# Kernel optimization log

Measured on AMD Instinct MI355X. Metric: run time of the kernel, lower is better.

Reference implementation:

```python
import jax, jax.numpy as jnp
import numpy as np

B, S, H = 2, 2048, 2048
NH, NKV, D = 32, 8, 64
N_REP = NH // NKV  # 4
THETA = 10000.0


def _rotate_half(x):
    x1, x2 = jnp.split(x, 2, axis=-1)
    return jnp.concatenate([-x2, x1], axis=-1)


def _apply_rope(q, k, position_ids):
    # q: [B,NH,S,D], k: [B,NKV,S,D], position_ids: [B,S]
    inv_freq = 1.0 / (THETA ** (jnp.arange(0, D, 2, dtype=jnp.float32) / D))  # [D/2]
    ang = position_ids[:, None, :, None].astype(jnp.float32) * inv_freq      # [B,1,S,D/2]
    cos = jnp.concatenate([jnp.cos(ang), jnp.cos(ang)], axis=-1)             # [B,1,S,D]
    sin = jnp.concatenate([jnp.sin(ang), jnp.sin(ang)], axis=-1)
    q = q * cos + _rotate_half(q) * sin
    k = k * cos + _rotate_half(k) * sin
    return q, k


def setup_inputs() -> dict:
    key = jax.random.key(0)
    k1, k2, k3, k4 = jax.random.split(key, 4)
    hidden_states = jax.random.normal(k1, (B, S, H), dtype=jnp.float32)
    position_ids = jnp.broadcast_to(jnp.arange(S, dtype=jnp.int64 if jax.config.jax_enable_x64 else jnp.int32)[None, :], (B, S))
    Wq = jax.random.normal(k2, (H, NH * D), dtype=jnp.float32) * 0.02
    Wkv = jax.random.normal(k3, (H, NKV * 2 * D), dtype=jnp.float32) * 0.02
    Wo = jax.random.normal(k4, (H, H), dtype=jnp.float32) * 0.02
    return {"hidden_states": hidden_states, "position_ids": position_ids,
            "Wq": Wq, "Wkv": Wkv, "Wo": Wo}


def reference(hidden_states, position_ids, Wq, Wkv, Wo):
    b, s, _ = hidden_states.shape
    # fused QKV projections (Linear, no bias)
    q = (hidden_states @ Wq).reshape(b, s, NH, D).transpose(0, 2, 1, 3)      # [B,NH,S,D]
    kv = (hidden_states @ Wkv).reshape(b, s, NKV, 2, D)
    k = kv[:, :, :, 0, :].transpose(0, 2, 1, 3)                              # [B,NKV,S,D]
    v = kv[:, :, :, 1, :].transpose(0, 2, 1, 3)                              # [B,NKV,S,D]
    # rotary embedding
    q, k = _apply_rope(q, k, position_ids)
    # GQA: repeat_interleave K/V heads
    k = jnp.repeat(k, N_REP, axis=1)                                         # [B,NH,S,D]
    v = jnp.repeat(v, N_REP, axis=1)
    # causal SDPA (eval mode: dropout_p = 0)
    scale = 1.0 / np.sqrt(D)
    scores = jnp.einsum('bhqd,bhkd->bhqk', q, k) * scale                     # [B,NH,S,S]
    causal = jnp.tril(jnp.ones((s, s), dtype=bool))
    scores = jnp.where(causal[None, None], scores, jnp.finfo(scores.dtype).min)
    probs = jax.nn.softmax(scores, axis=-1)
    ctx = jnp.einsum('bhqk,bhkd->bhqd', probs, v)                            # [B,NH,S,D]
    ctx = ctx.transpose(0, 2, 1, 3).reshape(b, s, H)
    return ctx @ Wo
```

## Files before the change

kernel.cpp:

```cpp
#include <hip/hip_runtime.h>

typedef __bf16 bf16_t;
typedef __bf16 bf16x8 __attribute__((ext_vector_type(8)));
typedef __bf16 bf16x4 __attribute__((ext_vector_type(4)));
typedef float f32x4 __attribute__((ext_vector_type(4)));

#define DEV static __device__ __forceinline__

DEV void gload16(const void* g, void* lds) {
  __builtin_amdgcn_global_load_lds((__attribute__((address_space(1))) void*)g,
                                   (__attribute__((address_space(3))) void*)lds, 16, 0, 0);
}

DEV f32x4 mfma16(bf16x8 a, bf16x8 b, f32x4 c) {
  return __builtin_amdgcn_mfma_f32_16x16x32_bf16(a, b, c, 0, 0, 0);
}

__global__ __launch_bounds__(256) void k_cvt_bf16(const float* __restrict__ in,
                                                  bf16_t* __restrict__ out, int n) {
  int i = (blockIdx.x * 256 + threadIdx.x) * 4;
  if (i + 3 < n) {
    float4 v = *(const float4*)(in + i);
    bf16x4 o;
    o[0] = (bf16_t)v.x; o[1] = (bf16_t)v.y; o[2] = (bf16_t)v.z; o[3] = (bf16_t)v.w;
    *(bf16x4*)(out + i) = o;
  }
}

__global__ __launch_bounds__(256) void k_transpose(const float* __restrict__ in,
                                                   bf16_t* __restrict__ out, int R, int C) {
  __shared__ float tile[32][33];
  const int tx = threadIdx.x & 31, ty = threadIdx.x >> 5;
  const int rb = blockIdx.y * 32, cb = blockIdx.x * 32;
#pragma unroll
  for (int i = 0; i < 32; i += 8)
    tile[ty + i][tx] = in[(size_t)(rb + ty + i) * C + (cb + tx)];
  __syncthreads();
#pragma unroll
  for (int i = 0; i < 32; i += 8)
    out[(size_t)(cb + ty + i) * R + (rb + tx)] = (bf16_t)tile[tx][ty + i];
}

__global__ __launch_bounds__(256) void k_rope_table(const int* __restrict__ pos_ids,
                                                    float2* __restrict__ tbl) {
  const int token = blockIdx.x * 8 + (threadIdx.x >> 5);
  const int d2 = threadIdx.x & 31;
  const float p = (float)pos_ids[token];
  const float freq = exp2f(-(float)d2 / 32.0f * log2f(10000.0f));
  const float a = p * freq;
  tbl[token * 32 + d2] = make_float2(cosf(a), sinf(a));
}

__global__ __launch_bounds__(256) void k_gemm_bt(const bf16_t* __restrict__ A,
                                                 const bf16_t* __restrict__ Bt,
                                                 float* __restrict__ C,
                                                 int M, int N, int K,
                                                 int lda, int ldb, int ldc) {
  __shared__ __align__(16) bf16_t As[128 * 32];
  __shared__ __align__(16) bf16_t Bs[128 * 32];
  const int tid = threadIdx.x;
  const int lane = tid & 63, w = tid >> 6;
  const int c15 = lane & 15, g = lane >> 4;
  const int wr = w >> 1, wc = w & 1;
  const int brow = blockIdx.y * 128, bcol = blockIdx.x * 128;
  const int swzr = (c15 >> 1) & 3;

  const f32x4 fzero = {0.f, 0.f, 0.f, 0.f};
  f32x4 acc[4][4];
#pragma unroll
  for (int m = 0; m < 4; ++m)
#pragma unroll
    for (int n = 0; n < 4; ++n) acc[m][n] = fzero;

  for (int kt = 0; kt < K; kt += 32) {
    __syncthreads();
#pragma unroll
    for (int i = 0; i < 2; ++i) {
      const int c = tid + i * 256;
      const int row = c >> 2, pc = c & 3;
      const int lc = pc ^ ((row >> 1) & 3);
      gload16(A + (size_t)(brow + row) * lda + kt + lc * 8,
              As + (size_t)(w * 64 + i * 256) * 8);
      gload16(Bt + (size_t)(bcol + row) * ldb + kt + lc * 8,
              Bs + (size_t)(w * 64 + i * 256) * 8);
    }
    __syncthreads();
    bf16x8 af[4], bfm[4];
#pragma unroll
    for (int m = 0; m < 4; ++m) {
      const int row = wr * 64 + m * 16 + c15;
      af[m] = *(const bf16x8*)(As + row * 32 + (g ^ swzr) * 8);
    }
#pragma unroll
    for (int n = 0; n < 4; ++n) {
      const int row = wc * 64 + n * 16 + c15;
      bfm[n] = *(const bf16x8*)(Bs + row * 32 + (g ^ swzr) * 8);
    }
#pragma unroll
    for (int m = 0; m < 4; ++m)
#pragma unroll
      for (int n = 0; n < 4; ++n)
        acc[m][n] = mfma16(af[m], bfm[n], acc[m][n]);
  }
#pragma unroll
  for (int m = 0; m < 4; ++m)
#pragma unroll
    for (int n = 0; n < 4; ++n)
#pragma unroll
      for (int r = 0; r < 4; ++r) {
        const int row = brow + wr * 64 + m * 16 + g * 4 + r;
        const int col = bcol + wc * 64 + n * 16 + c15;
        C[(size_t)row * ldc + col] = acc[m][n][r];
      }
}

__global__ __launch_bounds__(256) void k_gemm_qkv(const bf16_t* __restrict__ A,
                                                  const bf16_t* __restrict__ Bt,
                                                  const float2* __restrict__ tbl,
                                                  bf16_t* __restrict__ Qp,
                                                  bf16_t* __restrict__ Kp,
                                                  bf16_t* __restrict__ Vt) {
  __shared__ __align__(16) bf16_t As[128 * 32];
  __shared__ __align__(16) bf16_t Bs[128 * 32];
  const int tid = threadIdx.x;
  const int lane = tid & 63, w = tid >> 6;
  const int c15 = lane & 15, g = lane >> 4;
  const int wr = w >> 1, wc = w & 1;
  const int brow = blockIdx.y * 128, bcol = blockIdx.x * 128;
  const int swzr = (c15 >> 1) & 3;

  const f32x4 fzero = {0.f, 0.f, 0.f, 0.f};
  f32x4 acc[4][4];
#pragma unroll
  for (int m = 0; m < 4; ++m)
#pragma unroll
    for (int n = 0; n < 4; ++n) acc[m][n] = fzero;

  for (int kt = 0; kt < 2048; kt += 32) {
    __syncthreads();
#pragma unroll
    for (int i = 0; i < 2; ++i) {
      const int c = tid + i * 256;
      const int row = c >> 2, pc = c & 3;
      const int lc = pc ^ ((row >> 1) & 3);
      gload16(A + (size_t)(brow + row) * 2048 + kt + lc * 8,
              As + (size_t)(w * 64 + i * 256) * 8);
      gload16(Bt + (size_t)(bcol + row) * 2048 + kt + lc * 8,
              Bs + (size_t)(w * 64 + i * 256) * 8);
    }
    __syncthreads();
    bf16x8 af[4], bfm[4];
#pragma unroll
    for (int m = 0; m < 4; ++m) {
      const int row = wr * 64 + m * 16 + c15;
      af[m] = *(const bf16x8*)(As + row * 32 + (g ^ swzr) * 8);
    }
#pragma unroll
    for (int n = 0; n < 4; ++n) {
      const int row = wc * 64 + n * 16 + c15;
      bfm[n] = *(const bf16x8*)(Bs + row * 32 + (g ^ swzr) * 8);
    }
#pragma unroll
    for (int m = 0; m < 4; ++m)
#pragma unroll
      for (int n = 0; n < 4; ++n)
        acc[m][n] = mfma16(af[m], bfm[n], acc[m][n]);
  }

  const int seg = bcol + wc * 64;
  const int wrow = brow + wr * 64;
  const float QSCALE = 0.125f * 1.44269504088896340736f;

  if (seg < 2048) {
    const int hq = seg >> 6;
#pragma unroll
    for (int m = 0; m < 4; ++m)
#pragma unroll
      for (int r = 0; r < 4; ++r) {
        const int row = wrow + m * 16 + g * 4 + r;
        const int bb = row >> 11, s = row & 2047;
        const float2 cs0 = tbl[row * 32 + c15];
        const float2 cs1 = tbl[row * 32 + 16 + c15];
        bf16_t* dst = Qp + (((size_t)bb * 32 + hq) * 2048 + s) * 64;
        dst[c15]      = (bf16_t)((acc[m][0][r] * cs0.x - acc[m][2][r] * cs0.y) * QSCALE);
        dst[32 + c15] = (bf16_t)((acc[m][2][r] * cs0.x + acc[m][0][r] * cs0.y) * QSCALE);
        dst[16 + c15] = (bf16_t)((acc[m][1][r] * cs1.x - acc[m][3][r] * cs1.y) * QSCALE);
        dst[48 + c15] = (bf16_t)((acc[m][3][r] * cs1.x + acc[m][1][r] * cs1.y) * QSCALE);
      }
  } else {
    const int cc = seg - 2048;
    const int kvh = cc >> 7;
    if (((cc >> 6) & 1) == 0) {
#pragma unroll
      for (int m = 0; m < 4; ++m)
#pragma unroll
        for (int r = 0; r < 4; ++r) {
          const int row = wrow + m * 16 + g * 4 + r;
          const int bb = row >> 11, s = row & 2047;
          const float2 cs0 = tbl[row * 32 + c15];
          const float2 cs1 = tbl[row * 32 + 16 + c15];
          bf16_t* dst = Kp + (((size_t)bb * 8 + kvh) * 2048 + s) * 64;
          dst[c15]      = (bf16_t)(acc[m][0][r] * cs0.x - acc[m][2][r] * cs0.y);
          dst[32 + c15] = (bf16_t)(acc[m][2][r] * cs0.x + acc[m][0][r] * cs0.y);
          dst[16 + c15] = (bf16_t)(acc[m][1][r] * cs1.x - acc[m][3][r] * cs1.y);
          dst[48 + c15] = (bf16_t)(acc[m][3][r] * cs1.x + acc[m][1][r] * cs1.y);
        }
    } else {
#pragma unroll
      for (int m = 0; m < 4; ++m) {
        const int row0 = wrow + m * 16 + g * 4;
        const int bb = row0 >> 11, s0 = row0 & 2047;
#pragma unroll
        for (int n = 0; n < 4; ++n) {
          bf16x4 o;
#pragma unroll
          for (int r = 0; r < 4; ++r) o[r] = (bf16_t)acc[m][n][r];
          const int d = n * 16 + c15;
          *(bf16x4*)(Vt + ((size_t)(bb * 8 + kvh) * 64 + d) * 2048 + s0) = o;
        }
      }
    }
  }
}

__global__ __launch_bounds__(256, 3) void k_attn(const bf16_t* __restrict__ Qp,
                                                 const bf16_t* __restrict__ Kp,
                                                 const bf16_t* __restrict__ Vt,
                                                 bf16_t* __restrict__ ctx) {
  const int wgid = blockIdx.x;
  const int gidx = wgid & 15;
  const int j    = wgid >> 4;
  const int b = gidx >> 3, kvh = gidx & 7;
  const int qs = 63 - j;
  const int tid = threadIdx.x, lane = tid & 63, w = tid >> 6;
  const int h = kvh * 4 + w;
  const int c15 = lane & 15, g = lane >> 4;

  __shared__ __align__(16) bf16_t Ks[2][64 * 64];
  __shared__ __align__(16) bf16_t Vs[2][64 * 64];
  __shared__ __align__(16) bf16_t Pw[4][32 * 64];
  bf16_t* pw = &Pw[w][0];

  const int q0 = qs * 32;

  bf16x8 aq[2][2];
#pragma unroll
  for (int m = 0; m < 2; ++m) {
    const bf16_t* Qrow = Qp + (((size_t)b * 32 + h) * 2048 + q0 + m * 16 + c15) * 64;
    aq[m][0] = *(const bf16x8*)(Qrow + g * 8);
    aq[m][1] = *(const bf16x8*)(Qrow + 32 + g * 8);
  }
  asm volatile("s_waitcnt vmcnt(0)" ::: "memory");

  const bf16_t* Kb = Kp + ((size_t)b * 8 + kvh) * (size_t)(2048 * 64);
  const bf16_t* Vb = Vt + ((size_t)b * 8 + kvh) * (size_t)(64 * 2048);

  const int c0 = tid,      r0 = c0 >> 3, l0 = (c0 & 7) ^ (r0 & 7);
  const int c1 = tid + 256, r1 = c1 >> 3, l1 = (c1 & 7) ^ (r1 & 7);
  const int dst0 = (w * 64) * 8, dst1 = (w * 64 + 256) * 8;

  const f32x4 fzero = {0.f, 0.f, 0.f, 0.f};
  f32x4 acc[2][4];
  f32x4 lsum[2];
#pragma unroll
  for (int m = 0; m < 2; ++m) {
    lsum[m] = fzero;
#pragma unroll
    for (int n = 0; n < 4; ++n) acc[m][n] = fzero;
  }
  bf16x8 bones;
#pragma unroll
  for (int j2 = 0; j2 < 8; ++j2) bones[j2] = (bf16_t)1.0f;

  const int ntw = qs / 2 + 1;

  gload16(Kb + (size_t)r0 * 64 + l0 * 8, &Ks[0][dst0]);
  gload16(Kb + (size_t)r1 * 64 + l1 * 8, &Ks[0][dst1]);
  gload16(Vb + (size_t)r0 * 2048 + l0 * 8, &Vs[0][dst0]);
  gload16(Vb + (size_t)r1 * 2048 + l1 * 8, &Vs[0][dst1]);

  for (int t = 0; t < ntw; ++t) {
    const int kvbase = t * 64;
    const int tnb = (t + 1 < ntw ? t + 1 : t) * 64;
    const int nb = (t + 1) & 1, cb = t & 1;

    gload16(Kb + (size_t)(tnb + r0) * 64 + l0 * 8, &Ks[nb][dst0]);
    gload16(Kb + (size_t)(tnb + r1) * 64 + l1 * 8, &Ks[nb][dst1]);
    gload16(Vb + (size_t)r0 * 2048 + tnb + l0 * 8, &Vs[nb][dst0]);
    gload16(Vb + (size_t)r1 * 2048 + tnb + l1 * 8, &Vs[nb][dst1]);
    asm volatile("s_waitcnt vmcnt(4)" ::: "memory");
    __builtin_amdgcn_s_barrier();

    const bf16_t* Kc = &Ks[cb][0];
    f32x4 sv[2][4];
    __builtin_amdgcn_s_setprio(1);
#pragma unroll
    for (int n = 0; n < 4; ++n) {
      const int row = n * 16 + c15;
      const bf16x8 bk0 = *(const bf16x8*)(Kc + row * 64 + ((g ^ (row & 7)) << 3));
      const bf16x8 bk1 = *(const bf16x8*)(Kc + row * 64 + (((4 + g) ^ (row & 7)) << 3));
      sv[0][n] = mfma16(aq[0][1], bk1, mfma16(aq[0][0], bk0, fzero));
      sv[1][n] = mfma16(aq[1][1], bk1, mfma16(aq[1][0], bk0, fzero));
    }
    __builtin_amdgcn_s_setprio(0);

    if (kvbase + 63 > q0) {
#pragma unroll
      for (int n = 0; n < 4; ++n)
#pragma unroll
        for (int r = 0; r < 4; ++r) {
          const int col = kvbase + n * 16 + c15;
          if (col > q0 + g * 4 + r)      sv[0][n][r] = -1e30f;
          if (col > q0 + 16 + g * 4 + r) sv[1][n][r] = -1e30f;
        }
    }
#pragma unroll
    for (int n = 0; n < 4; ++n)
#pragma unroll
      for (int r = 0; r < 4; ++r) {
        const int col = n * 16 + c15;
        const int rp0 = g * 4 + r, rp1 = 16 + g * 4 + r;
        pw[rp0 * 64 + ((((col >> 3) ^ (rp0 & 7)) << 3) | (col & 7))] = (bf16_t)exp2f(sv[0][n][r]);
        pw[rp1 * 64 + ((((col >> 3) ^ (rp1 & 7)) << 3) | (col & 7))] = (bf16_t)exp2f(sv[1][n][r]);
      }
    asm volatile("s_waitcnt lgkmcnt(0)" ::: "memory");
    __builtin_amdgcn_sched_barrier(0);

    bf16x8 ap[2][2];
#pragma unroll
    for (int m = 0; m < 2; ++m) {
      const int q = m * 16 + c15;
      ap[m][0] = *(const bf16x8*)(pw + q * 64 + ((g ^ (q & 7)) << 3));
      ap[m][1] = *(const bf16x8*)(pw + q * 64 + (((4 + g) ^ (q & 7)) << 3));
    }
    const bf16_t* Vc = &Vs[cb][0];
    __builtin_amdgcn_s_setprio(1);
#pragma unroll
    for (int m = 0; m < 2; ++m)
      lsum[m] = mfma16(ap[m][1], bones, mfma16(ap[m][0], bones, lsum[m]));
#pragma unroll
    for (int n = 0; n < 4; ++n) {
      const int row = n * 16 + c15;
      const bf16x8 bv0 = *(const bf16x8*)(Vc + row * 64 + ((g ^ (row & 7)) << 3));
      const bf16x8 bv1 = *(const bf16x8*)(Vc + row * 64 + (((4 + g) ^ (row & 7)) << 3));
#pragma unroll
      for (int m = 0; m < 2; ++m)
        acc[m][n] = mfma16(ap[m][1], bv1, mfma16(ap[m][0], bv0, acc[m][n]));
    }
    __builtin_amdgcn_s_setprio(0);
    __builtin_amdgcn_s_barrier();
  }

#pragma unroll
  for (int m = 0; m < 2; ++m) {
    float inv[4];
#pragma unroll
    for (int r = 0; r < 4; ++r) inv[r] = 1.0f / lsum[m][r];
#pragma unroll
    for (int n = 0; n < 4; ++n)
#pragma unroll
      for (int r = 0; r < 4; ++r) {
        const int rowq = q0 + m * 16 + g * 4 + r;
        const int col = h * 64 + n * 16 + c15;
        ctx[((size_t)b * 2048 + rowq) * 2048 + col] = (bf16_t)(acc[m][n][r] * inv[r]);
      }
  }
}

extern "C" void kernel_launch(void* const* d_in, const int* in_sizes, int n_in,
                              void* d_out, int out_size, void* d_ws, size_t ws_size,
                              hipStream_t stream) {
  const float* hs  = (const float*)d_in[0];
  const int*   pos = (const int*)d_in[1];
  const float* Wq  = (const float*)d_in[2];
  const float* Wkv = (const float*)d_in[3];
  const float* Wo  = (const float*)d_in[4];
  float* out = (float*)d_out;
  (void)in_sizes; (void)n_in; (void)out_size; (void)ws_size;

  char* p = (char*)d_ws;
  bf16_t* Xbf   = (bf16_t*)p; p += (size_t)4096 * 2048 * 2;
  bf16_t* Wqkvt = (bf16_t*)p; p += (size_t)3072 * 2048 * 2;
  bf16_t* Wot   = (bf16_t*)p; p += (size_t)2048 * 2048 * 2;
  float2* tbl   = (float2*)p; p += (size_t)4096 * 32 * 8;
  bf16_t* Qp    = (bf16_t*)p; p += (size_t)2 * 32 * 2048 * 64 * 2;
  bf16_t* Kp    = (bf16_t*)p; p += (size_t)2 * 8 * 2048 * 64 * 2;
  bf16_t* Vt    = (bf16_t*)p; p += (size_t)2 * 8 * 64 * 2048 * 2;
  bf16_t* ctx   = (bf16_t*)p; p += (size_t)4096 * 2048 * 2;

  k_cvt_bf16<<<8192, 256, 0, stream>>>(hs, Xbf, 4096 * 2048);
  k_transpose<<<dim3(64, 64), 256, 0, stream>>>(Wq, Wqkvt, 2048, 2048);
  k_transpose<<<dim3(32, 64), 256, 0, stream>>>(Wkv, Wqkvt + (size_t)2048 * 2048, 2048, 1024);
  k_transpose<<<dim3(64, 64), 256, 0, stream>>>(Wo, Wot, 2048, 2048);
  k_rope_table<<<512, 256, 0, stream>>>(pos, tbl);
  k_gemm_qkv<<<dim3(24, 32), 256, 0, stream>>>(Xbf, Wqkvt, tbl, Qp, Kp, Vt);
  k_attn<<<1024, 256, 0, stream>>>(Qp, Kp, Vt, ctx);
  k_gemm_bt<<<dim3(16, 32), 256, 0, stream>>>(ctx, Wot, out,
                                              4096, 2048, 2048, 2048, 2048, 2048);
}
```

Measured before the change: 232.4 us.

## Replace GEMMs with 256x256 double-buffered, phase-scheduled MFMA kernel

Both projection GEMMs (QKV with fused RoPE epilogue, and output projection) move to one templated 256x256-tile, 512-thread kernel. It uses 64-wide K stages, double-buffered LDS, async global-to-LDS prefetch two stages ahead, s_setprio/barrier phasing, and XCD-aware block remapping. The aim is to cut global traffic per FLOP and hide load latency behind MFMA work. In exchange it uses more registers and LDS and launches fewer blocks (192 and 128), which may underfill the 256 CUs.

```diff
diff --git a/kernel.cpp b/kernel.cpp
--- a/kernel.cpp
+++ b/kernel.cpp
@@ -51,172 +51,187 @@
   tbl[token * 32 + d2] = make_float2(cosf(a), sinf(a));
 }
 
-__global__ __launch_bounds__(256) void k_gemm_bt(const bf16_t* __restrict__ A,
-                                                 const bf16_t* __restrict__ Bt,
-                                                 float* __restrict__ C,
-                                                 int M, int N, int K,
-                                                 int lda, int ldb, int ldc) {
-  __shared__ __align__(16) bf16_t As[128 * 32];
-  __shared__ __align__(16) bf16_t Bs[128 * 32];
+#define STAGE_A(bi, st, h)                                                      \
+  do {                                                                          \
+    const bf16_t* _s = gA + (size_t)(brow + (h) * 128 + r0) * gK + (st) * 64 + l0 * 8; \
+    gload16(_s, &As[bi][((h) * 1024 + tid) * 8]);                               \
+    gload16(_s + (size_t)64 * gK, &As[bi][((h) * 1024 + 512 + tid) * 8]);       \
+  } while (0)
+
+#define STAGE_B(bi, st, h)                                                      \
+  do {                                                                          \
+    const bf16_t* _s = gB + (size_t)(bcol + (h) * 128 + r0) * gK + (st) * 64 + l0 * 8; \
+    gload16(_s, &Bs[bi][((h) * 1024 + tid) * 8]);                               \
+    gload16(_s + (size_t)64 * gK, &Bs[bi][((h) * 1024 + 512 + tid) * 8]);       \
+  } while (0)
+
+#define LOADA(bi, mh)                                                           \
+  _Pragma("unroll")                                                             \
+  for (int mq = 0; mq < 4; ++mq) {                                              \
+    const int R = wm * 128 + (mh) * 64 + mq * 16 + c15;                         \
+    af[mq][0] = *(const bf16x8*)(&As[bi][(R * 8 + (g ^ (R & 7))) * 8]);         \
+    af[mq][1] = *(const bf16x8*)(&As[bi][(R * 8 + ((4 + g) ^ (R & 7))) * 8]);   \
+  }
+
+#define LOADB(bi, nh)                                                           \
+  _Pragma("unroll")                                                             \
+  for (int nq = 0; nq < 2; ++nq) {                                              \
+    const int R = wn * 64 + ((nh) * 2 + nq) * 16 + c15;                         \
+    bfr[nq][0] = *(const bf16x8*)(&Bs[bi][(R * 8 + (g ^ (R & 7))) * 8]);        \
+    bfr[nq][1] = *(const bf16x8*)(&Bs[bi][(R * 8 + ((4 + g) ^ (R & 7))) * 8]);  \
+  }
+
+#define MFMAQ(mh, nh)                                                           \
+  _Pragma("unroll")                                                             \
+  for (int nq = 0; nq < 2; ++nq)                                                \
+    _Pragma("unroll")                                                           \
+    for (int mq = 0; mq < 4; ++mq)                                              \
+      acc[(mh) * 4 + mq][(nh) * 2 + nq] =                                       \
+          mfma16(af[mq][1], bfr[nq][1],                                         \
+                 mfma16(af[mq][0], bfr[nq][0], acc[(mh) * 4 + mq][(nh) * 2 + nq]));
+
+#define PH_MID()                                            \
+  __builtin_amdgcn_s_barrier();                             \
+  asm volatile("s_waitcnt lgkmcnt(0)" ::: "memory");        \
+  __builtin_amdgcn_sched_barrier(0);                        \
+  __builtin_amdgcn_s_setprio(1)
+
+#define PH_END()                                            \
+  __builtin_amdgcn_s_setprio(0);                            \
+  __builtin_amdgcn_s_barrier()
+
+template <int MODE>
+__global__ __launch_bounds__(512, 2) void k_gemm256(
+    const bf16_t* __restrict__ gA, const bf16_t* __restrict__ gB,
+    int gK, int NBX,
+    float* __restrict__ C, int ldc,
+    const float2* __restrict__ tbl,
+    bf16_t* __restrict__ Qp, bf16_t* __restrict__ Kp, bf16_t* __restrict__ Vt) {
+  __shared__ __align__(16) bf16_t As[2][256 * 64];
+  __shared__ __align__(16) bf16_t Bs[2][256 * 64];
   const int tid = threadIdx.x;
   const int lane = tid & 63, w = tid >> 6;
   const int c15 = lane & 15, g = lane >> 4;
-  const int wr = w >> 1, wc = w & 1;
-  const int brow = blockIdx.y * 128, bcol = blockIdx.x * 128;
-  const int swzr = (c15 >> 1) & 3;
+  const int wm = w >> 2, wn = w & 3;
+
+  const int cpx = (int)gridDim.x >> 3;
+  const int u = ((int)blockIdx.x & 7) * cpx + ((int)blockIdx.x >> 3);
+  const int bx = u % NBX, by = u / NBX;
+  const int brow = by * 256, bcol = bx * 256;
+
+  const int r0 = tid >> 3, p0 = tid & 7;
+  const int l0 = p0 ^ (r0 & 7);
 
   const f32x4 fzero = {0.f, 0.f, 0.f, 0.f};
-  f32x4 acc[4][4];
-#pragma unroll
-  for (int m = 0; m < 4; ++m)
+  f32x4 acc[8][4];
+#pragma unroll
+  for (int m = 0; m < 8; ++m)
 #pragma unroll
     for (int n = 0; n < 4; ++n) acc[m][n] = fzero;
 
-  for (int kt = 0; kt < K; kt += 32) {
-    __syncthreads();
-#pragma unroll
-    for (int i = 0; i < 2; ++i) {
-      const int c = tid + i * 256;
-      const int row = c >> 2, pc = c & 3;
-      const int lc = pc ^ ((row >> 1) & 3);
-      gload16(A + (size_t)(brow + row) * lda + kt + lc * 8,
-              As + (size_t)(w * 64 + i * 256) * 8);
-      gload16(Bt + (size_t)(bcol + row) * ldb + kt + lc * 8,
-              Bs + (size_t)(w * 64 + i * 256) * 8);
-    }
-    __syncthreads();
-    bf16x8 af[4], bfm[4];
-#pragma unroll
-    for (int m = 0; m < 4; ++m) {
-      const int row = wr * 64 + m * 16 + c15;
-      af[m] = *(const bf16x8*)(As + row * 32 + (g ^ swzr) * 8);
-    }
-#pragma unroll
-    for (int n = 0; n < 4; ++n) {
-      const int row = wc * 64 + n * 16 + c15;
-      bfm[n] = *(const bf16x8*)(Bs + row * 32 + (g ^ swzr) * 8);
-    }
-#pragma unroll
-    for (int m = 0; m < 4; ++m)
+  const int NT = gK >> 6;
+
+  STAGE_A(0, 0, 0); STAGE_A(0, 0, 1); STAGE_B(0, 0, 0); STAGE_B(0, 0, 1);
+  STAGE_A(1, 1, 0);
+  asm volatile("s_waitcnt vmcnt(2)" ::: "memory");
+  __builtin_amdgcn_s_barrier();
+
+  for (int t = 0; t < NT; ++t) {
+    const int bi = t & 1, oi = bi ^ 1;
+    const int st1 = (t + 1 < NT) ? t + 1 : NT - 1;
+    const int st2 = (t + 2 < NT) ? t + 2 : NT - 1;
+    bf16x8 af[4][2], bfr[2][2];
+
+    LOADA(bi, 0);
+    LOADB(bi, 0);
+    STAGE_A(oi, st1, 1);
+    STAGE_B(oi, st1, 0);
+    PH_MID();
+    MFMAQ(0, 0);
+    PH_END();
+
+    LOADB(bi, 1);
+    STAGE_B(oi, st1, 1);
+    PH_MID();
+    MFMAQ(0, 1);
+    PH_END();
+
+    LOADA(bi, 1);
+    LOADB(bi, 0);
+    PH_MID();
+    MFMAQ(1, 0);
+    PH_END();
+
+    LOADB(bi, 1);
+    STAGE_A(bi, st2, 0);
+    asm volatile("s_waitcnt vmcnt(2)" ::: "memory");
+    PH_MID();
+    MFMAQ(1, 1);
+    PH_END();
+  }
+
+  if constexpr (MODE == 0) {
+#pragma unroll
+    for (int m = 0; m < 8; ++m)
 #pragma unroll
       for (int n = 0; n < 4; ++n)
-        acc[m][n] = mfma16(af[m], bfm[n], acc[m][n]);
-  }
-#pragma unroll
-  for (int m = 0; m < 4; ++m)
-#pragma unroll
-    for (int n = 0; n < 4; ++n)
-#pragma unroll
-      for (int r = 0; r < 4; ++r) {
-        const int row = brow + wr * 64 + m * 16 + g * 4 + r;
-        const int col = bcol + wc * 64 + n * 16 + c15;
-        C[(size_t)row * ldc + col] = acc[m][n][r];
-      }
-}
-
-__global__ __launch_bounds__(256) void k_gemm_qkv(const bf16_t* __restrict__ A,
-                                                  const bf16_t* __restrict__ Bt,
-                                                  const float2* __restrict__ tbl,
-                                                  bf16_t* __restrict__ Qp,
-                                                  bf16_t* __restrict__ Kp,
-                                                  bf16_t* __restrict__ Vt) {
-  __shared__ __align__(16) bf16_t As[128 * 32];
-  __shared__ __align__(16) bf16_t Bs[128 * 32];
-  const int tid = threadIdx.x;
-  const int lane = tid & 63, w = tid >> 6;
-  const int c15 = lane & 15, g = lane >> 4;
-  const int wr = w >> 1, wc = w & 1;
-  const int brow = blockIdx.y * 128, bcol = blockIdx.x * 128;
-  const int swzr = (c15 >> 1) & 3;
-
-  const f32x4 fzero = {0.f, 0.f, 0.f, 0.f};
-  f32x4 acc[4][4];
-#pragma unroll
-  for (int m = 0; m < 4; ++m)
-#pragma unroll
-    for (int n = 0; n < 4; ++n) acc[m][n] = fzero;
-
-  for (int kt = 0; kt < 2048; kt += 32) {
-    __syncthreads();
-#pragma unroll
-    for (int i = 0; i < 2; ++i) {
-      const int c = tid + i * 256;
-      const int row = c >> 2, pc = c & 3;
-      const int lc = pc ^ ((row >> 1) & 3);
-      gload16(A + (size_t)(brow + row) * 2048 + kt + lc * 8,
-              As + (size_t)(w * 64 + i * 256) * 8);
-      gload16(Bt + (size_t)(bcol + row) * 2048 + kt + lc * 8,
-              Bs + (size_t)(w * 64 + i * 256) * 8);
-    }
-    __syncthreads();
-    bf16x8 af[4], bfm[4];
-#pragma unroll
-    for (int m = 0; m < 4; ++m) {
-      const int row = wr * 64 + m * 16 + c15;
-      af[m] = *(const bf16x8*)(As + row * 32 + (g ^ swzr) * 8);
-    }
-#pragma unroll
-    for (int n = 0; n < 4; ++n) {
-      const int row = wc * 64 + n * 16 + c15;
-      bfm[n] = *(const bf16x8*)(Bs + row * 32 + (g ^ swzr) * 8);
-    }
-#pragma unroll
-    for (int m = 0; m < 4; ++m)
-#pragma unroll
-      for (int n = 0; n < 4; ++n)
-        acc[m][n] = mfma16(af[m], bfm[n], acc[m][n]);
-  }
-
-  const int seg = bcol + wc * 64;
-  const int wrow = brow + wr * 64;
-  const float QSCALE = 0.125f * 1.44269504088896340736f;
-
-  if (seg < 2048) {
-    const int hq = seg >> 6;
-#pragma unroll
-    for (int m = 0; m < 4; ++m)
-#pragma unroll
-      for (int r = 0; r < 4; ++r) {
-        const int row = wrow + m * 16 + g * 4 + r;
-        const int bb = row >> 11, s = row & 2047;
-        const float2 cs0 = tbl[row * 32 + c15];
-        const float2 cs1 = tbl[row * 32 + 16 + c15];
-        bf16_t* dst = Qp + (((size_t)bb * 32 + hq) * 2048 + s) * 64;
-        dst[c15]      = (bf16_t)((acc[m][0][r] * cs0.x - acc[m][2][r] * cs0.y) * QSCALE);
-        dst[32 + c15] = (bf16_t)((acc[m][2][r] * cs0.x + acc[m][0][r] * cs0.y) * QSCALE);
-        dst[16 + c15] = (bf16_t)((acc[m][1][r] * cs1.x - acc[m][3][r] * cs1.y) * QSCALE);
-        dst[48 + c15] = (bf16_t)((acc[m][3][r] * cs1.x + acc[m][1][r] * cs1.y) * QSCALE);
-      }
+#pragma unroll
+        for (int r = 0; r < 4; ++r) {
+          const int row = brow + wm * 128 + m * 16 + g * 4 + r;
+          const int col = bcol + wn * 64 + n * 16 + c15;
+          C[(size_t)row * ldc + col] = acc[m][n][r];
+        }
   } else {
-    const int cc = seg - 2048;
-    const int kvh = cc >> 7;
-    if (((cc >> 6) & 1) == 0) {
-#pragma unroll
-      for (int m = 0; m < 4; ++m)
+    const int seg = bcol + wn * 64;
+    const int wrow = brow + wm * 128;
+    const float QSCALE = 0.125f * 1.44269504088896340736f;
+    if (seg < 2048) {
+      const int hq = seg >> 6;
+#pragma unroll
+      for (int m = 0; m < 8; ++m)
 #pragma unroll
         for (int r = 0; r < 4; ++r) {
           const int row = wrow + m * 16 + g * 4 + r;
           const int bb = row >> 11, s = row & 2047;
           const float2 cs0 = tbl[row * 32 + c15];
           const float2 cs1 = tbl[row * 32 + 16 + c15];
-          bf16_t* dst = Kp + (((size_t)bb * 8 + kvh) * 2048 + s) * 64;
-          dst[c15]      = (bf16_t)(acc[m][0][r] * cs0.x - acc[m][2][r] * cs0.y);
-          dst[32 + c15] = (bf16_t)(acc[m][2][r] * cs0.x + acc[m][0][r] * cs0.y);
-          dst[16 + c15] = (bf16_t)(acc[m][1][r] * cs1.x - acc[m][3][r] * cs1.y);
-          dst[48 + c15] = (bf16_t)(acc[m][3][r] * cs1.x + acc[m][1][r] * cs1.y);
+          bf16_t* dst = Qp + (((size_t)bb * 32 + hq) * 2048 + s) * 64;
+          dst[c15]      = (bf16_t)((acc[m][0][r] * cs0.x - acc[m][2][r] * cs0.y) * QSCALE);
+          dst[32 + c15] = (bf16_t)((acc[m][2][r] * cs0.x + acc[m][0][r] * cs0.y) * QSCALE);
+          dst[16 + c15] = (bf16_t)((acc[m][1][r] * cs1.x - acc[m][3][r] * cs1.y) * QSCALE);
+          dst[48 + c15] = (bf16_t)((acc[m][3][r] * cs1.x + acc[m][1][r] * cs1.y) * QSCALE);
         }
     } else {
-#pragma unroll
-      for (int m = 0; m < 4; ++m) {
-        const int row0 = wrow + m * 16 + g * 4;
-        const int bb = row0 >> 11, s0 = row0 & 2047;
-#pragma unroll
-        for (int n = 0; n < 4; ++n) {
-          bf16x4 o;
-#pragma unroll
-          for (int r = 0; r < 4; ++r) o[r] = (bf16_t)acc[m][n][r];
-          const int d = n * 16 + c15;
-          *(bf16x4*)(Vt + ((size_t)(bb * 8 + kvh) * 64 + d) * 2048 + s0) = o;
+      const int cc = seg - 2048;
+      const int kvh = cc >> 7;
+      if (((cc >> 6) & 1) == 0) {
+#pragma unroll
+        for (int m = 0; m < 8; ++m)
+#pragma unroll
+          for (int r = 0; r < 4; ++r) {
+            const int row = wrow + m * 16 + g * 4 + r;
+            const int bb = row >> 11, s = row & 2047;
+            const float2 cs0 = tbl[row * 32 + c15];
+            const float2 cs1 = tbl[row * 32 + 16 + c15];
+            bf16_t* dst = Kp + (((size_t)bb * 8 + kvh) * 2048 + s) * 64;
+            dst[c15]      = (bf16_t)(acc[m][0][r] * cs0.x - acc[m][2][r] * cs0.y);
+            dst[32 + c15] = (bf16_t)(acc[m][2][r] * cs0.x + acc[m][0][r] * cs0.y);
+            dst[16 + c15] = (bf16_t)(acc[m][1][r] * cs1.x - acc[m][3][r] * cs1.y);
+            dst[48 + c15] = (bf16_t)(acc[m][3][r] * cs1.x + acc[m][1][r] * cs1.y);
+          }
+      } else {
+#pragma unroll
+        for (int m = 0; m < 8; ++m) {
+          const int row0 = wrow + m * 16 + g * 4;
+          const int bb = row0 >> 11, s0 = row0 & 2047;
+#pragma unroll
+          for (int n = 0; n < 4; ++n) {
+            bf16x4 o;
+#pragma unroll
+            for (int r = 0; r < 4; ++r) o[r] = (bf16_t)acc[m][n][r];
+            const int d = n * 16 + c15;
+            *(bf16x4*)(Vt + ((size_t)(bb * 8 + kvh) * 64 + d) * 2048 + s0) = o;
+          }
         }
       }
     }
@@ -393,8 +408,9 @@
   k_transpose<<<dim3(32, 64), 256, 0, stream>>>(Wkv, Wqkvt + (size_t)2048 * 2048, 2048, 1024);
   k_transpose<<<dim3(64, 64), 256, 0, stream>>>(Wo, Wot, 2048, 2048);
   k_rope_table<<<512, 256, 0, stream>>>(pos, tbl);
-  k_gemm_qkv<<<dim3(24, 32), 256, 0, stream>>>(Xbf, Wqkvt, tbl, Qp, Kp, Vt);
+  k_gemm256<1><<<192, 512, 0, stream>>>(Xbf, Wqkvt, 2048, 12,
+                                        nullptr, 0, tbl, Qp, Kp, Vt);
   k_attn<<<1024, 256, 0, stream>>>(Qp, Kp, Vt, ctx);
-  k_gemm_bt<<<dim3(16, 32), 256, 0, stream>>>(ctx, Wot, out,
-                                              4096, 2048, 2048, 2048, 2048, 2048);
-}
+  k_gemm256<0><<<128, 512, 0, stream>>>(ctx, Wot, 2048, 8,
+                                        out, 2048, nullptr, nullptr, nullptr, nullptr);
+}
```

Result: faster. 214.9 us (-7.5%).
